# Kernel tuning notes

Hardware: AMD Instinct MI355X
Metric: run time of the kernel (lower is better)

## Reference

```python
import jax, jax.numpy as jnp
import numpy as np

LAYERS = 2      # LightGCN propagation layers
LAMB = 0.5      # aux loss weight
REG = 1e-4      # embedding reg weight
N_AUX = 2       # len(behaviors) - 1


def setup_inputs() -> dict:
    key = jax.random.key(0)
    k = jax.random.split(key, 8)
    n_users, n_items, d = 100000, 50000, 32
    E = 1000000
    user_emb = (jax.random.normal(k[0], (n_users + 1, d), jnp.float32) * 0.1).at[0].set(0.0)
    item_emb = (jax.random.normal(k[1], (n_items + 1, d), jnp.float32) * 0.1).at[0].set(0.0)
    aux_u = jax.random.randint(k[2], (N_AUX, E), 1, n_users + 1)
    aux_i = jax.random.randint(k[3], (N_AUX, E), 1, n_items + 1)
    aux_edges = jnp.stack([aux_u, aux_i], axis=-1).astype(jnp.int32)
    tgt_u = jax.random.randint(k[4], (E,), 1, n_users + 1)
    tgt_i = jax.random.randint(k[5], (E,), 1, n_items + 1)
    target_edges = jnp.stack([tgt_u, tgt_i], axis=-1).astype(jnp.int32)
    # [B, 1+N_AUX, 3]: per row (user, pos_item, neg_item) for target then each aux behavior
    batch_data = jax.random.randint(k[6], (4096, 1 + N_AUX, 3), 1, n_items + 1).astype(jnp.int32)
    return {"user_emb": user_emb, "item_emb": item_emb, "batch_data": batch_data,
            "aux_edges": aux_edges, "target_edges": target_edges}


def _graph(edges, n_user_rows, N):
    """Symmetric-normalized bipartite LightGCN graph as directed COO (src, dst, w)."""
    u = edges[:, 0]
    v = edges[:, 1] + n_user_rows  # shift item ids into joint node space
    ones = jnp.ones(u.shape[0], jnp.float32)
    deg = jax.ops.segment_sum(ones, u, num_segments=N) + jax.ops.segment_sum(ones, v, num_segments=N)
    dinv = jnp.where(deg > 0, jax.lax.rsqrt(jnp.maximum(deg, 1.0)), 0.0)
    w = dinv[u] * dinv[v]
    src = jnp.concatenate([u, v])
    dst = jnp.concatenate([v, u])
    w2 = jnp.concatenate([w, w])
    return src, dst, w2


def _lightgcn(emb, src, dst, w, N):
    """L-layer LightGCN propagation, mean over layers 0..L."""
    acc = emb
    cur = emb
    for _ in range(LAYERS):
        cur = jax.ops.segment_sum(w[:, None] * cur[src], dst, num_segments=N)
        acc = acc + cur
    return acc / (LAYERS + 1)


def _prob(ue, ie, u, i):
    return jax.nn.relu(jnp.sum(ue[u] * ie[i], axis=-1))


def _bpr(p, n):
    return -jnp.mean(jax.nn.log_sigmoid(p - n))


def reference(user_emb, item_emb, batch_data, aux_edges, target_edges):
    Nu = user_emb.shape[0]
    N = Nu + item_emb.shape[0]
    all_emb = jnp.concatenate([user_emb, item_emb], axis=0)
    tgt_g = _graph(target_edges, Nu, N)

    user, p_item, n_item = batch_data[:, 0, 0], batch_data[:, 0, 1], batch_data[:, 0, 2]
    aux_user, aux_p, aux_n = batch_data[:, 1:, 0], batch_data[:, 1:, 1], batch_data[:, 1:, 2]

    cps, cns, dps, dns, aps, ans, aux_losses = [], [], [], [], [], [], []
    for idx in range(N_AUX):
        # combine graph = aux behavior edges union target edges
        comb_edges = jnp.concatenate([aux_edges[idx], target_edges], axis=0)
        ce = _lightgcn(all_emb, *_graph(comb_edges, Nu, N), N)
        cu, ci = ce[:Nu], ce[Nu:]
        cps.append(_prob(cu, ci, user, p_item))
        cns.append(_prob(cu, ci, user, n_item))

        ae = _lightgcn(all_emb, *_graph(aux_edges[idx], Nu, N), N)
        au, ai = ae[:Nu], ae[Nu:]
        aps.append(_prob(au, ai, user, p_item))
        ans.append(_prob(au, ai, user, n_item))

        # condition: propagate aux embeddings through the target graph
        de = _lightgcn(ae, *tgt_g, N)
        du, di = de[:Nu], de[Nu:]
        dps.append(_prob(du, di, user, p_item))
        dns.append(_prob(du, di, user, n_item))

        ps = jnp.sum(au[aux_user[:, idx]] * ai[aux_p[:, idx]], axis=-1)
        ns = jnp.sum(au[aux_user[:, idx]] * ai[aux_n[:, idx]], axis=-1)
        aux_losses.append(_bpr(ps, ns))

    aux_loss = jnp.mean(jnp.stack(aux_losses))

    def front_door(cond, comb, aux):
        return jnp.sum(cond * jnp.sum(comb * aux, axis=0), axis=0)

    p_scores = front_door(jnp.stack(dps), jnp.stack(cps), jnp.stack(aps))
    n_scores = front_door(jnp.stack(dns), jnp.stack(cns), jnp.stack(ans))
    rec_loss = _bpr(p_scores, n_scores)
    emb_loss = (jnp.linalg.norm(user_emb) + jnp.linalg.norm(item_emb)) / item_emb.shape[0]
    return rec_loss + LAMB * aux_loss + REG * emb_loss
```

## Files before the change

### kernel.cpp

```cpp
#include <hip/hip_runtime.h>
#include <math.h>

#define D 32
#define ROWU 16
#define NBK 1024
#define BSHIFT 8
#define TILE_H 16384
#define TILE_BIN 2048
#define BCAP 7680

typedef unsigned int u32;
typedef unsigned short u16;

__device__ __forceinline__ float logsigf(float x) {
  return fminf(x, 0.f) - log1pf(expf(-fabsf(x)));
}

__device__ __forceinline__ float lo16(u32 u) { return __uint_as_float(u << 16); }
__device__ __forceinline__ float hi16(u32 u) { return __uint_as_float(u & 0xFFFF0000u); }
__device__ __forceinline__ u32 pk2(float a, float b) {
  u32 ua = __float_as_uint(a), ub = __float_as_uint(b);
  u32 ra = (ua + 0x7FFFu + ((ua >> 16) & 1u)) >> 16;
  u32 rb = (ub + 0x7FFFu + ((ub >> 16) & 1u)) >> 16;
  return (ra & 0xFFFFu) | (rb << 16);
}
__device__ __forceinline__ float bfat(const u16* __restrict__ p, size_t off) {
  return __uint_as_float(((u32)p[off]) << 16);
}
__device__ __forceinline__ void accum8(float* a, float w, uint4 x) {
  a[0] += w * lo16(x.x); a[1] += w * hi16(x.x);
  a[2] += w * lo16(x.y); a[3] += w * hi16(x.y);
  a[4] += w * lo16(x.z); a[5] += w * hi16(x.z);
  a[6] += w * lo16(x.w); a[7] += w * hi16(x.w);
}
__device__ __forceinline__ uint4 pack8(const float* a, float w) {
  return make_uint4(pk2(w * a[0], w * a[1]), pk2(w * a[2], w * a[3]),
                    pk2(w * a[4], w * a[5]), pk2(w * a[6], w * a[7]));
}


__global__ void hist_kernel(const int2* __restrict__ tgt, const int2* __restrict__ aux,
                            int E, int Nu, int BPS, int* __restrict__ bcur) {
  __shared__ int lh[NBK];
  int seg = blockIdx.x / BPS;
  int blk = blockIdx.x - seg * BPS;
  const int2* edges = (seg == 0) ? tgt : aux + (size_t)(seg - 1) * E;
  for (int b = threadIdx.x; b < NBK; b += 256) lh[b] = 0;
  __syncthreads();
  int e0 = blk * TILE_H;
  for (int k = threadIdx.x; k < TILE_H; k += 256) {
    int e = e0 + k;
    if (e < E) {
      int2 ed = edges[e];
      atomicAdd(&lh[ed.x >> BSHIFT], 1);
      atomicAdd(&lh[(ed.y + Nu) >> BSHIFT], 1);
    }
  }
  __syncthreads();
  for (int b = threadIdx.x; b < NBK; b += 256)
    if (lh[b]) atomicAdd(&bcur[seg * NBK + b], lh[b]);
}

__global__ void bscan_kernel(int* __restrict__ bcur) {
  int* b = bcur + blockIdx.x * NBK;
  int lane = threadIdx.x;
  int carry = 0;
  for (int base = 0; base < NBK; base += 64) {
    int i = base + lane;
    int v = b[i];
    int s = v;
    #pragma unroll
    for (int o = 1; o < 64; o <<= 1) {
      int t = __shfl_up(s, o);
      if (lane >= o) s += t;
    }
    b[i] = carry + s - v;
    carry += __shfl(s, 63);
  }
}

__global__ void bin_kernel(const int2* __restrict__ tgt, const int2* __restrict__ aux,
                           int E, int Nu, int BPS, int* __restrict__ bcur,
                           int* __restrict__ binned) {
  __shared__ int stage[2 * TILE_BIN];
  __shared__ int lh[NBK];
  __shared__ int loff[NBK];
  __shared__ int gb[NBK];
  __shared__ int wred[4];
  __shared__ int stot;
  int seg = blockIdx.x / BPS;
  int blk = blockIdx.x - seg * BPS;
  const int2* edges = (seg == 0) ? tgt : aux + (size_t)(seg - 1) * E;
  int* out = binned + (size_t)seg * 2 * E;
  int tid = threadIdx.x;
  for (int b = tid; b < NBK; b += 256) lh[b] = 0;
  __syncthreads();
  int e0 = blk * TILE_BIN;
  int pkv[16];
  int pb[16];
  int pr[16];
  #pragma unroll
  for (int it = 0; it < 8; ++it) {
    int e = e0 + tid + it * 256;
    bool ok = e < E;
    int2 ed = ok ? edges[e] : make_int2(0, -Nu);
    int u = ed.x, v = ed.y + Nu;
    int b1 = u >> BSHIFT, b2 = v >> BSHIFT;
    pkv[2 * it] = ((u & 255) << 18) | v;
    pb[2 * it] = b1;
    pr[2 * it] = ok ? atomicAdd(&lh[b1], 1) : 0;
    pkv[2 * it + 1] = ((v & 255) << 18) | u;
    pb[2 * it + 1] = b2;
    pr[2 * it + 1] = ok ? atomicAdd(&lh[b2], 1) : 0;
  }
  __syncthreads();
  int lane = tid & 63, wid = tid >> 6;
  int b4 = tid * 4;
  int v0 = lh[b4], v1 = lh[b4 + 1], v2 = lh[b4 + 2], v3 = lh[b4 + 3];
  int tsum = v0 + v1 + v2 + v3;
  int incl = tsum;
  #pragma unroll
  for (int o = 1; o < 64; o <<= 1) {
    int t = __shfl_up(incl, o);
    if (lane >= o) incl += t;
  }
  if (lane == 63) wred[wid] = incl;
  __syncthreads();
  int wbase = 0;
  for (int w = 0; w < wid; ++w) wbase += wred[w];
  int excl = wbase + incl - tsum;
  loff[b4] = excl;
  loff[b4 + 1] = excl + v0;
  loff[b4 + 2] = excl + v0 + v1;
  loff[b4 + 3] = excl + v0 + v1 + v2;
  if (tid == 255) stot = excl + tsum;
  #pragma unroll
  for (int j = 0; j < 4; ++j) {
    int b = b4 + j;
    int c = lh[b];
    gb[b] = c ? atomicAdd(&bcur[seg * NBK + b], c) : 0;
  }
  __syncthreads();
  #pragma unroll
  for (int it = 0; it < 16; ++it) {
    int e = e0 + tid + (it >> 1) * 256;
    if (e < E) stage[loff[pb[it]] + pr[it]] = pkv[it];
  }
  __syncthreads();
  int tot = stot;
  for (int k = tid; k < tot; k += 256) {
    int lo = 0, hi = NBK;
    while (lo < hi) {
      int mid = (lo + hi) >> 1;
      if (loff[mid] <= k) lo = mid + 1; else hi = mid;
    }
    int b = lo - 1;
    out[gb[b] + (k - loff[b])] = stage[k];
  }
}

__global__ void bucket_csr_kernel(const int* __restrict__ binned,
                                  const int* __restrict__ bend, int E2, int N, int NBKe,
                                  int* __restrict__ deg3, int* __restrict__ rp3,
                                  int* __restrict__ col_all) {
  __shared__ int ent[BCAP];
  __shared__ int cnt[256];
  __shared__ int off[256];
  __shared__ int wred[4];
  int seg = blockIdx.x / NBKe;
  int bkt = blockIdx.x - seg * NBKe;
  int node0 = bkt << BSHIFT;
  const int* bc = bend + seg * NBK;
  int start = (bkt == 0) ? 0 : bc[bkt - 1];
  int end = bc[bkt];
  int cntE = end - start;
  const int* src = binned + (size_t)seg * E2 + start;
  bool inLds = (cntE <= BCAP);
  if (inLds)
    for (int k = threadIdx.x; k < cntE; k += 256) ent[k] = src[k];
  cnt[threadIdx.x] = 0;
  __syncthreads();
  for (int k = threadIdx.x; k < cntE; k += 256) {
    int en = inLds ? ent[k] : src[k];
    atomicAdd(&cnt[en >> 18], 1);
  }
  __syncthreads();
  int lane = threadIdx.x & 63, wid = threadIdx.x >> 6;
  int v = cnt[threadIdx.x];
  int incl = v;
  #pragma unroll
  for (int o = 1; o < 64; o <<= 1) {
    int t = __shfl_up(incl, o);
    if (lane >= o) incl += t;
  }
  if (lane == 63) wred[wid] = incl;
  __syncthreads();
  int wbase = 0;
  for (int w = 0; w < wid; ++w) wbase += wred[w];
  off[threadIdx.x] = wbase + incl - v;
  int node = node0 + (int)threadIdx.x;
  if (node < N) {
    deg3[(size_t)seg * N + node] = v;
    rp3[(size_t)seg * (N + 1) + node] = start + wbase + incl - v;
  }
  if (bkt == 0 && threadIdx.x == 0) rp3[(size_t)seg * (N + 1) + N] = E2;
  __syncthreads();
  cnt[threadIdx.x] = 0;
  __syncthreads();
  int* col = col_all + (size_t)seg * E2 + start;
  for (int k = threadIdx.x; k < cntE; k += 256) {
    int en = inLds ? ent[k] : src[k];
    int lb = en >> 18;
    int pos = atomicAdd(&cnt[lb], 1);
    col[off[lb] + pos] = en & 0x3FFFF;
  }
}

__global__ void dinv_all_kernel(const int* __restrict__ deg3, float* __restrict__ dinv5,
                                int N) {
  int n = blockIdx.x * blockDim.x + threadIdx.x;
  if (n >= N) return;
  int dt = deg3[n], d0 = deg3[N + n], d1 = deg3[2 * N + n];
  dinv5[n]         = dt ? rsqrtf((float)dt) : 0.f;
  dinv5[N + n]     = d0 ? rsqrtf((float)d0) : 0.f;
  dinv5[2 * N + n] = d1 ? rsqrtf((float)d1) : 0.f;
  int c0 = dt + d0, c1 = dt + d1;
  dinv5[3 * N + n] = c0 ? rsqrtf((float)c0) : 0.f;
  dinv5[4 * N + n] = c1 ? rsqrtf((float)c1) : 0.f;
}

__global__ void cvt_emb_kernel(const float2* __restrict__ ue, long nu2,
                               const float2* __restrict__ ie, long ni2,
                               u32* __restrict__ emb) {
  long i = (long)blockIdx.x * blockDim.x + threadIdx.x;
  if (i >= nu2 + ni2) return;
  float2 v = (i < nu2) ? ue[i] : ie[i - nu2];
  emb[i] = pk2(v.x, v.y);
}


__global__ void gather_fused_all_kernel(const int* __restrict__ rp3,
                                        const int* __restrict__ col_all,
                                        const float* __restrict__ dinv5,
                                        const uint4* __restrict__ emb,
                                        uint4* __restrict__ BaAll, uint4* __restrict__ BcAll,
                                        int N, int E2) {
  const int* rpA0 = rp3 + (size_t)1 * (N + 1);
  const int* rpA1 = rp3 + (size_t)2 * (N + 1);
  const int* colA0 = col_all + (size_t)1 * E2;
  const int* colA1 = col_all + (size_t)2 * E2;
  const float* dvA0 = dinv5 + (size_t)1 * N;
  const float* dvA1 = dinv5 + (size_t)2 * N;
  const float* dvC0 = dinv5 + (size_t)3 * N;
  const float* dvC1 = dinv5 + (size_t)4 * N;
  int t = blockIdx.x * blockDim.x + threadIdx.x;
  int n = t >> 2;
  if (n >= N) return;
  int lane = t & 3;
  float aA0[8] = {0, 0, 0, 0, 0, 0, 0, 0};
  float aA1[8] = {0, 0, 0, 0, 0, 0, 0, 0};
  float aC0[8] = {0, 0, 0, 0, 0, 0, 0, 0};
  float aC1[8] = {0, 0, 0, 0, 0, 0, 0, 0};
  int s = rpA0[n], e = rpA0[n + 1];
  int j = s;
  for (; j + 1 < e; j += 2) {
    int c0 = colA0[j], c1 = colA0[j + 1];
    float wa0 = dvA0[c0], wc0 = dvC0[c0];
    float wa1 = dvA0[c1], wc1 = dvC0[c1];
    uint4 x0 = emb[(size_t)c0 * 4 + lane];
    uint4 x1 = emb[(size_t)c1 * 4 + lane];
    accum8(aA0, wa0, x0); accum8(aC0, wc0, x0);
    accum8(aA0, wa1, x1); accum8(aC0, wc1, x1);
  }
  if (j < e) {
    int c = colA0[j];
    float wa = dvA0[c], wc = dvC0[c];
    uint4 x = emb[(size_t)c * 4 + lane];
    accum8(aA0, wa, x); accum8(aC0, wc, x);
  }
  s = rpA1[n]; e = rpA1[n + 1];
  j = s;
  for (; j + 1 < e; j += 2) {
    int c0 = colA1[j], c1 = colA1[j + 1];
    float wa0 = dvA1[c0], wc0 = dvC1[c0];
    float wa1 = dvA1[c1], wc1 = dvC1[c1];
    uint4 x0 = emb[(size_t)c0 * 4 + lane];
    uint4 x1 = emb[(size_t)c1 * 4 + lane];
    accum8(aA1, wa0, x0); accum8(aC1, wc0, x0);
    accum8(aA1, wa1, x1); accum8(aC1, wc1, x1);
  }
  if (j < e) {
    int c = colA1[j];
    float wa = dvA1[c], wc = dvC1[c];
    uint4 x = emb[(size_t)c * 4 + lane];
    accum8(aA1, wa, x); accum8(aC1, wc, x);
  }
  s = rp3[n]; e = rp3[n + 1];
  j = s;
  for (; j + 1 < e; j += 2) {
    int c0 = col_all[j], c1 = col_all[j + 1];
    float w00 = dvC0[c0], w10 = dvC1[c0];
    float w01 = dvC0[c1], w11 = dvC1[c1];
    uint4 x0 = emb[(size_t)c0 * 4 + lane];
    uint4 x1 = emb[(size_t)c1 * 4 + lane];
    accum8(aC0, w00, x0); accum8(aC1, w10, x0);
    accum8(aC0, w01, x1); accum8(aC1, w11, x1);
  }
  if (j < e) {
    int c = col_all[j];
    float w0 = dvC0[c], w1 = dvC1[c];
    uint4 x = emb[(size_t)c * 4 + lane];
    accum8(aC0, w0, x); accum8(aC1, w1, x);
  }
  size_t o = (size_t)n * 4 + lane;
  size_t rowN4 = (size_t)N * 4;
  BaAll[o] = pack8(aA0, dvA0[n]);
  BaAll[rowN4 + o] = pack8(aA1, dvA1[n]);
  BcAll[o] = pack8(aC0, dvC0[n]);
  BcAll[rowN4 + o] = pack8(aC1, dvC1[n]);
}

__global__ void gather_avg_kernel(const int* __restrict__ rp3, const int* __restrict__ col_all,
                                  const float* __restrict__ dinv5,
                                  const uint4* __restrict__ emb,
                                  const uint4* __restrict__ BaAll, uint4* __restrict__ AAll,
                                  int N, int E2) {
  int idx = blockIdx.y;
  const int* rp = rp3 + (size_t)(1 + idx) * (N + 1);
  const int* col = col_all + (size_t)(1 + idx) * E2;
  const float* dv = dinv5 + (size_t)(1 + idx) * N;
  const uint4* cur = BaAll + (size_t)idx * N * 4;
  uint4* outA = AAll + (size_t)idx * N * 4;
  int t = blockIdx.x * blockDim.x + threadIdx.x;
  int n = t >> 2;
  if (n >= N) return;
  int lane = t & 3;
  float acc[8] = {0, 0, 0, 0, 0, 0, 0, 0};
  int s = rp[n], e = rp[n + 1];
  int j = s;
  for (; j + 1 < e; j += 2) {
    int c0 = col[j], c1 = col[j + 1];
    float w0 = dv[c0], w1 = dv[c1];
    uint4 x0 = cur[(size_t)c0 * 4 + lane];
    uint4 x1 = cur[(size_t)c1 * 4 + lane];
    accum8(acc, w0, x0);
    accum8(acc, w1, x1);
  }
  if (j < e) {
    int c = col[j];
    float w = dv[c];
    uint4 x = cur[(size_t)c * 4 + lane];
    accum8(acc, w, x);
  }
  float wn = dv[n];
  uint4 e4 = emb[(size_t)n * 4 + lane];
  uint4 b4 = cur[(size_t)n * 4 + lane];
  float r[8];
  r[0] = (lo16(e4.x) + lo16(b4.x) + wn * acc[0]) * (1.f / 3.f);
  r[1] = (hi16(e4.x) + hi16(b4.x) + wn * acc[1]) * (1.f / 3.f);
  r[2] = (lo16(e4.y) + lo16(b4.y) + wn * acc[2]) * (1.f / 3.f);
  r[3] = (hi16(e4.y) + hi16(b4.y) + wn * acc[3]) * (1.f / 3.f);
  r[4] = (lo16(e4.z) + lo16(b4.z) + wn * acc[4]) * (1.f / 3.f);
  r[5] = (hi16(e4.z) + hi16(b4.z) + wn * acc[5]) * (1.f / 3.f);
  r[6] = (lo16(e4.w) + lo16(b4.w) + wn * acc[6]) * (1.f / 3.f);
  r[7] = (hi16(e4.w) + hi16(b4.w) + wn * acc[7]) * (1.f / 3.f);
  outA[(size_t)n * 4 + lane] = pack8(r, 1.f);
}

__global__ void de_gather_kernel(const int* __restrict__ rp3, const int* __restrict__ col_all,
                                 const float* __restrict__ dinv5,
                                 const uint4* __restrict__ AAll, uint4* __restrict__ BaAll,
                                 int N, int E2) {
  int idx = blockIdx.y;
  const uint4* cur = AAll + (size_t)idx * N * 4;
  uint4* out = BaAll + (size_t)idx * N * 4;
  int t = blockIdx.x * blockDim.x + threadIdx.x;
  int n = t >> 2;
  if (n >= N) return;
  int lane = t & 3;
  float acc[8] = {0, 0, 0, 0, 0, 0, 0, 0};
  int s = rp3[n], e = rp3[n + 1];
  int j = s;
  for (; j + 1 < e; j += 2) {
    int c0 = col_all[j], c1 = col_all[j + 1];
    float w0 = dinv5[c0], w1 = dinv5[c1];
    uint4 x0 = cur[(size_t)c0 * 4 + lane];
    uint4 x1 = cur[(size_t)c1 * 4 + lane];
    accum8(acc, w0, x0);
    accum8(acc, w1, x1);
  }
  if (j < e) {
    int c = col_all[j];
    float w = dinv5[c];
    uint4 x = cur[(size_t)c * 4 + lane];
    accum8(acc, w, x);
  }
  out[(size_t)n * 4 + lane] = pack8(acc, dinv5[n]);
}


__device__ __forceinline__ float fdim2(const int* __restrict__ rpA, const int* __restrict__ colA,
                                       const int* __restrict__ rpT, const int* __restrict__ colT,
                                       const float* __restrict__ dv,
                                       const u16* __restrict__ base, const u16* __restrict__ L1,
                                       int r, int d) {
  float acc = 0.f;
  for (int j = rpA[r]; j < rpA[r + 1]; ++j) {
    int c = colA[j];
    acc += dv[c] * bfat(L1, (size_t)c * D + d);
  }
  if (colT != nullptr) {
    for (int j = rpT[r]; j < rpT[r + 1]; ++j) {
      int c = colT[j];
      acc += dv[c] * bfat(L1, (size_t)c * D + d);
    }
  }
  return (bfat(base, (size_t)r * D + d) + bfat(L1, (size_t)r * D + d) + dv[r] * acc) * (1.f / 3.f);
}

__global__ void ce_sparse_kernel(const int* __restrict__ rp3, const int* __restrict__ col_all,
                                 const float* __restrict__ dinv5,
                                 const u32* __restrict__ EMBu, const u32* __restrict__ BcAll,
                                 const int* __restrict__ batch, int Bsz, int Nu, int N, int E2,
                                 float* __restrict__ cps, float* __restrict__ cns) {
  int idx = blockIdx.y;
  const int* rpA = rp3 + (size_t)(1 + idx) * (N + 1);
  const int* colA = col_all + (size_t)(1 + idx) * E2;
  const float* dv = dinv5 + (size_t)(3 + idx) * N;
  const u16* base = (const u16*)EMBu;
  const u16* L1 = (const u16*)(BcAll + (size_t)idx * N * ROWU);
  float* outp = cps + (size_t)idx * Bsz;
  float* outn = cns + (size_t)idx * Bsz;
  int t = blockIdx.x * blockDim.x + threadIdx.x;
  int b = t >> 5, d = t & 31;
  if (b >= Bsz) return;
  int u = batch[b * 9 + 0];
  int p = batch[b * 9 + 1] + Nu;
  int n = batch[b * 9 + 2] + Nu;
  float uv = fdim2(rpA, colA, rp3, col_all, dv, base, L1, u, d);
  float pv = fdim2(rpA, colA, rp3, col_all, dv, base, L1, p, d);
  float nv = fdim2(rpA, colA, rp3, col_all, dv, base, L1, n, d);
  float sp = uv * pv, sn = uv * nv;
  #pragma unroll
  for (int o = 16; o > 0; o >>= 1) {
    sp += __shfl_down(sp, o, 32);
    sn += __shfl_down(sn, o, 32);
  }
  if (d == 0) {
    outp[b] = fmaxf(sp, 0.f);
    outn[b] = fmaxf(sn, 0.f);
  }
}

__global__ void de_sparse_kernel(const int* __restrict__ rp3, const int* __restrict__ col_all,
                                 const float* __restrict__ dinv5,
                                 const u32* __restrict__ AAll, const u32* __restrict__ BaAll,
                                 const int* __restrict__ batch, int Bsz, int Nu, int N, int E2,
                                 float* __restrict__ dps, float* __restrict__ dns) {
  int idx = blockIdx.y;
  const u16* base = (const u16*)(AAll + (size_t)idx * N * ROWU);
  const u16* L1 = (const u16*)(BaAll + (size_t)idx * N * ROWU);
  float* outp = dps + (size_t)idx * Bsz;
  float* outn = dns + (size_t)idx * Bsz;
  int t = blockIdx.x * blockDim.x + threadIdx.x;
  int b = t >> 5, d = t & 31;
  if (b >= Bsz) return;
  int u = batch[b * 9 + 0];
  int p = batch[b * 9 + 1] + Nu;
  int n = batch[b * 9 + 2] + Nu;
  float uv = fdim2(rp3, col_all, nullptr, nullptr, dinv5, base, L1, u, d);
  float pv = fdim2(rp3, col_all, nullptr, nullptr, dinv5, base, L1, p, d);
  float nv = fdim2(rp3, col_all, nullptr, nullptr, dinv5, base, L1, n, d);
  float sp = uv * pv, sn = uv * nv;
  #pragma unroll
  for (int o = 16; o > 0; o >>= 1) {
    sp += __shfl_down(sp, o, 32);
    sn += __shfl_down(sn, o, 32);
  }
  if (d == 0) {
    outp[b] = fmaxf(sp, 0.f);
    outn[b] = fmaxf(sn, 0.f);
  }
}


__device__ __forceinline__ float dotrow(const u32* __restrict__ a, const u32* __restrict__ b) {
  float s = 0.f;
  #pragma unroll
  for (int k = 0; k < ROWU; ++k) {
    u32 x = a[k], y = b[k];
    s += lo16(x) * lo16(y) + hi16(x) * hi16(y);
  }
  return s;
}

__global__ void score_aux_kernel(const u32* __restrict__ AAll, const int* __restrict__ batch,
                                 int Bsz, int Nu, int N, float* __restrict__ aps,
                                 float* __restrict__ ans_, float* __restrict__ accs) {
  int idx = blockIdx.y;
  const u32* A = AAll + (size_t)idx * N * ROWU;
  float* outp = aps + (size_t)idx * Bsz;
  float* outn = ans_ + (size_t)idx * Bsz;
  int b = blockIdx.x * blockDim.x + threadIdx.x;
  float l = 0.f;
  if (b < Bsz) {
    int u = batch[b * 9 + 0];
    int p = batch[b * 9 + 1] + Nu;
    int n = batch[b * 9 + 2] + Nu;
    const u32* ur = A + (size_t)u * ROWU;
    outp[b] = fmaxf(dotrow(ur, A + (size_t)p * ROWU), 0.f);
    outn[b] = fmaxf(dotrow(ur, A + (size_t)n * ROWU), 0.f);
    const int* r = batch + b * 9 + 3 * (1 + idx);
    const u32* aur = A + (size_t)r[0] * ROWU;
    float ps = dotrow(aur, A + (size_t)(r[1] + Nu) * ROWU);
    float ns = dotrow(aur, A + (size_t)(r[2] + Nu) * ROWU);
    l = -logsigf(ps - ns);
  }
  for (int o = 32; o > 0; o >>= 1) l += __shfl_down(l, o);
  if ((threadIdx.x & 63) == 0) atomicAdd(&accs[idx], l);
}

__global__ void recloss_kernel(const float* __restrict__ cps, const float* __restrict__ cns,
                               const float* __restrict__ aps, const float* __restrict__ ans_,
                               const float* __restrict__ dps, const float* __restrict__ dns,
                               int Bsz, int NA, float* __restrict__ acc) {
  int b = blockIdx.x * blockDim.x + threadIdx.x;
  float l = 0.f;
  if (b < Bsz) {
    float dp = 0.f, dn = 0.f, cap = 0.f, can = 0.f;
    for (int i = 0; i < NA; ++i) {
      dp += dps[i * Bsz + b];
      dn += dns[i * Bsz + b];
      cap += cps[i * Bsz + b] * aps[i * Bsz + b];
      can += cns[i * Bsz + b] * ans_[i * Bsz + b];
    }
    l = -logsigf(dp * cap - dn * can);
  }
  for (int o = 32; o > 0; o >>= 1) l += __shfl_down(l, o);
  if ((threadIdx.x & 63) == 0) atomicAdd(acc, l);
}

__global__ void sumsq2_kernel(const float4* __restrict__ xu, int n4u,
                              const float4* __restrict__ xi, int n4i,
                              float* __restrict__ accU, float* __restrict__ accI) {
  __shared__ float redU[4], redI[4];
  int tid = threadIdx.x;
  int gid = blockIdx.x * blockDim.x + tid;
  int stride = gridDim.x * blockDim.x;
  float su = 0.f, si = 0.f;
  for (int i = gid; i < n4u; i += stride) {
    float4 v = xu[i];
    su += v.x * v.x + v.y * v.y + v.z * v.z + v.w * v.w;
  }
  for (int i = gid; i < n4i; i += stride) {
    float4 v = xi[i];
    si += v.x * v.x + v.y * v.y + v.z * v.z + v.w * v.w;
  }
  for (int o = 32; o > 0; o >>= 1) {
    su += __shfl_down(su, o);
    si += __shfl_down(si, o);
  }
  if ((tid & 63) == 0) { redU[tid >> 6] = su; redI[tid >> 6] = si; }
  __syncthreads();
  if (tid == 0) {
    atomicAdd(accU, redU[0] + redU[1] + redU[2] + redU[3]);
    atomicAdd(accI, redI[0] + redI[1] + redI[2] + redI[3]);
  }
}

__global__ void final_kernel(const float* __restrict__ accs, int Bsz, int NA, int NiRows,
                             float* __restrict__ out) {
  float rec = accs[NA] / (float)Bsz;
  float aux = 0.f;
  for (int i = 0; i < NA; ++i) aux += accs[i] / (float)Bsz;
  aux /= (float)NA;
  float embl = (sqrtf(accs[NA + 1]) + sqrtf(accs[NA + 2])) / (float)NiRows;
  out[0] = rec + 0.5f * aux + 1e-4f * embl;
}

extern "C" void kernel_launch(void* const* d_in, const int* in_sizes, int n_in,
                              void* d_out, int out_size, void* d_ws, size_t ws_size,
                              hipStream_t stream) {
  const float* user_emb = (const float*)d_in[0];
  const float* item_emb = (const float*)d_in[1];
  const int* batch = (const int*)d_in[2];
  const int* aux_edges = (const int*)d_in[3];
  const int* tgt_edges = (const int*)d_in[4];

  const int NuRows = in_sizes[0] / D;
  const int NiRows = in_sizes[1] / D;
  const int Bsz = in_sizes[2] / 9;
  const int E = in_sizes[4] / 2;
  const int NA = in_sizes[3] / (2 * E);
  const int N = NuRows + NiRows;
  const int E2 = 2 * E;
  const size_t rowH = (size_t)N * ROWU;
  const int BPS_H = (E + TILE_H - 1) / TILE_H;
  const int BPS_B = (E + TILE_BIN - 1) / TILE_BIN;
  const int NBKe = (N + (1 << BSHIFT) - 1) >> BSHIFT;

  u32* EMBu = (u32*)d_ws;
  u32* AAll = EMBu + rowH;
  u32* BaAll = AAll + 2 * rowH;
  u32* BcAll = BaAll + 2 * rowH;
  int* deg3 = (int*)(BcAll + 2 * rowH);
  float* dinv5 = (float*)(deg3 + 3 * (size_t)N);
  int* rp3 = (int*)(dinv5 + 5 * (size_t)N);
  int* bcur = rp3 + 3 * (size_t)(N + 1);
  int* col_all = bcur + 3 * (size_t)NBK;
  float* cps = (float*)(col_all + 3 * (size_t)E2);
  float* cns = cps + (size_t)NA * Bsz;
  float* aps = cns + (size_t)NA * Bsz;
  float* ans_ = aps + (size_t)NA * Bsz;
  float* dps = ans_ + (size_t)NA * Bsz;
  float* dns = dps + (size_t)NA * Bsz;
  float* accs = dns + (size_t)NA * Bsz;
  int* binned = (int*)AAll;

  const int TB = 256;
  const int gN = (N + TB - 1) / TB;
  const int gN4 = (N * 4 + TB - 1) / TB;
  const int gB = (Bsz + TB - 1) / TB;
  const int gB32 = (Bsz * 32 + TB - 1) / TB;
  const long nu2 = (long)NuRows * ROWU;
  const long ni2 = (long)NiRows * ROWU;
  const int gCvt = (int)((nu2 + ni2 + TB - 1) / TB);

  cvt_emb_kernel<<<gCvt, TB, 0, stream>>>((const float2*)user_emb, nu2,
                                          (const float2*)item_emb, ni2, EMBu);

  hipMemsetAsync(bcur, 0, 3 * (size_t)NBK * sizeof(int), stream);
  hist_kernel<<<3 * BPS_H, TB, 0, stream>>>((const int2*)tgt_edges, (const int2*)aux_edges,
                                            E, NuRows, BPS_H, bcur);
  bscan_kernel<<<3, 64, 0, stream>>>(bcur);
  bin_kernel<<<3 * BPS_B, TB, 0, stream>>>((const int2*)tgt_edges, (const int2*)aux_edges,
                                           E, NuRows, BPS_B, bcur, binned);
  bucket_csr_kernel<<<3 * NBKe, TB, 0, stream>>>(binned, bcur, E2, N, NBKe,
                                                 deg3, rp3, col_all);
  dinv_all_kernel<<<gN, TB, 0, stream>>>(deg3, dinv5, N);

  hipMemsetAsync(accs, 0, (size_t)(NA + 3) * sizeof(float), stream);

  dim3 gridG(gN4, NA), gridB(gB, NA), gridS(gB32, NA);

  gather_fused_all_kernel<<<gN4, TB, 0, stream>>>(rp3, col_all, dinv5, (const uint4*)EMBu,
                                                  (uint4*)BaAll, (uint4*)BcAll, N, E2);
  gather_avg_kernel<<<gridG, TB, 0, stream>>>(rp3, col_all, dinv5, (const uint4*)EMBu,
                                              (const uint4*)BaAll, (uint4*)AAll, N, E2);
  score_aux_kernel<<<gridB, TB, 0, stream>>>(AAll, batch, Bsz, NuRows, N, aps, ans_, accs);
  ce_sparse_kernel<<<gridS, TB, 0, stream>>>(rp3, col_all, dinv5, EMBu, BcAll,
                                             batch, Bsz, NuRows, N, E2, cps, cns);
  de_gather_kernel<<<gridG, TB, 0, stream>>>(rp3, col_all, dinv5, (const uint4*)AAll,
                                             (uint4*)BaAll, N, E2);
  de_sparse_kernel<<<gridS, TB, 0, stream>>>(rp3, col_all, dinv5, AAll, BaAll,
                                             batch, Bsz, NuRows, N, E2, dps, dns);

  sumsq2_kernel<<<104, TB, 0, stream>>>((const float4*)user_emb,
                                        (int)((size_t)NuRows * D / 4),
                                        (const float4*)item_emb,
                                        (int)((size_t)NiRows * D / 4),
                                        accs + NA + 1, accs + NA + 2);
  recloss_kernel<<<gB, TB, 0, stream>>>(cps, cns, aps, ans_, dps, dns, Bsz, NA, accs + NA);
  final_kernel<<<1, 1, 0, stream>>>(accs, Bsz, NA, NiRows, (float*)d_out);
}
```

Measured before the change: 683.3 us.

## Interleave both aux embeddings per node and fuse de_gather across behaviors

The aux-propagated embeddings for both behaviors are now stored interleaved per node (64 bf16 per row), so the target-graph gather runs once with 8 lanes per node instead of once per behavior. The CSR column and weight lookups for the target graph are shared across both behaviors, and each neighbor fetch reads one contiguous 128-byte row. The gather_avg inner loop is also unrolled by four to put more loads in flight. Score and sparse kernels are updated to index the interleaved layout, at the cost of strided writes in gather_avg.

Measured after the change: 651.1 us. -4.7%, faster.

```diff
diff --git a/kernel.cpp b/kernel.cpp
--- a/kernel.cpp
+++ b/kernel.cpp
@@ -323,14 +323,13 @@
 __global__ void gather_avg_kernel(const int* __restrict__ rp3, const int* __restrict__ col_all,
                                   const float* __restrict__ dinv5,
                                   const uint4* __restrict__ emb,
-                                  const uint4* __restrict__ BaAll, uint4* __restrict__ AAll,
+                                  const uint4* __restrict__ BaAll, uint4* __restrict__ AI,
                                   int N, int E2) {
   int idx = blockIdx.y;
   const int* rp = rp3 + (size_t)(1 + idx) * (N + 1);
   const int* col = col_all + (size_t)(1 + idx) * E2;
   const float* dv = dinv5 + (size_t)(1 + idx) * N;
   const uint4* cur = BaAll + (size_t)idx * N * 4;
-  uint4* outA = AAll + (size_t)idx * N * 4;
   int t = blockIdx.x * blockDim.x + threadIdx.x;
   int n = t >> 2;
   if (n >= N) return;
@@ -338,15 +337,19 @@
   float acc[8] = {0, 0, 0, 0, 0, 0, 0, 0};
   int s = rp[n], e = rp[n + 1];
   int j = s;
-  for (; j + 1 < e; j += 2) {
-    int c0 = col[j], c1 = col[j + 1];
-    float w0 = dv[c0], w1 = dv[c1];
+  for (; j + 3 < e; j += 4) {
+    int c0 = col[j], c1 = col[j + 1], c2 = col[j + 2], c3 = col[j + 3];
+    float w0 = dv[c0], w1 = dv[c1], w2 = dv[c2], w3 = dv[c3];
     uint4 x0 = cur[(size_t)c0 * 4 + lane];
     uint4 x1 = cur[(size_t)c1 * 4 + lane];
+    uint4 x2 = cur[(size_t)c2 * 4 + lane];
+    uint4 x3 = cur[(size_t)c3 * 4 + lane];
     accum8(acc, w0, x0);
     accum8(acc, w1, x1);
-  }
-  if (j < e) {
+    accum8(acc, w2, x2);
+    accum8(acc, w3, x3);
+  }
+  for (; j < e; ++j) {
     int c = col[j];
     float w = dv[c];
     uint4 x = cur[(size_t)c * 4 + lane];
@@ -364,38 +367,35 @@
   r[5] = (hi16(e4.z) + hi16(b4.z) + wn * acc[5]) * (1.f / 3.f);
   r[6] = (lo16(e4.w) + lo16(b4.w) + wn * acc[6]) * (1.f / 3.f);
   r[7] = (hi16(e4.w) + hi16(b4.w) + wn * acc[7]) * (1.f / 3.f);
-  outA[(size_t)n * 4 + lane] = pack8(r, 1.f);
+  AI[(size_t)n * 8 + idx * 4 + lane] = pack8(r, 1.f);
 }
 
 __global__ void de_gather_kernel(const int* __restrict__ rp3, const int* __restrict__ col_all,
                                  const float* __restrict__ dinv5,
-                                 const uint4* __restrict__ AAll, uint4* __restrict__ BaAll,
-                                 int N, int E2) {
-  int idx = blockIdx.y;
-  const uint4* cur = AAll + (size_t)idx * N * 4;
-  uint4* out = BaAll + (size_t)idx * N * 4;
+                                 const uint4* __restrict__ AI, uint4* __restrict__ DeI,
+                                 int N) {
   int t = blockIdx.x * blockDim.x + threadIdx.x;
-  int n = t >> 2;
+  int n = t >> 3;
   if (n >= N) return;
-  int lane = t & 3;
+  int lane = t & 7;
   float acc[8] = {0, 0, 0, 0, 0, 0, 0, 0};
   int s = rp3[n], e = rp3[n + 1];
   int j = s;
   for (; j + 1 < e; j += 2) {
     int c0 = col_all[j], c1 = col_all[j + 1];
     float w0 = dinv5[c0], w1 = dinv5[c1];
-    uint4 x0 = cur[(size_t)c0 * 4 + lane];
-    uint4 x1 = cur[(size_t)c1 * 4 + lane];
+    uint4 x0 = AI[(size_t)c0 * 8 + lane];
+    uint4 x1 = AI[(size_t)c1 * 8 + lane];
     accum8(acc, w0, x0);
     accum8(acc, w1, x1);
   }
   if (j < e) {
     int c = col_all[j];
     float w = dinv5[c];
-    uint4 x = cur[(size_t)c * 4 + lane];
+    uint4 x = AI[(size_t)c * 8 + lane];
     accum8(acc, w, x);
   }
-  out[(size_t)n * 4 + lane] = pack8(acc, dinv5[n]);
+  DeI[(size_t)n * 8 + lane] = pack8(acc, dinv5[n]);
 }
 
 
@@ -409,13 +409,23 @@
     int c = colA[j];
     acc += dv[c] * bfat(L1, (size_t)c * D + d);
   }
-  if (colT != nullptr) {
-    for (int j = rpT[r]; j < rpT[r + 1]; ++j) {
-      int c = colT[j];
-      acc += dv[c] * bfat(L1, (size_t)c * D + d);
-    }
+  for (int j = rpT[r]; j < rpT[r + 1]; ++j) {
+    int c = colT[j];
+    acc += dv[c] * bfat(L1, (size_t)c * D + d);
   }
   return (bfat(base, (size_t)r * D + d) + bfat(L1, (size_t)r * D + d) + dv[r] * acc) * (1.f / 3.f);
+}
+
+__device__ __forceinline__ float fdim1i(const int* __restrict__ rp, const int* __restrict__ col,
+                                        const float* __restrict__ dv,
+                                        const u16* __restrict__ base, const u16* __restrict__ L1,
+                                        int r, int di) {
+  float acc = 0.f;
+  for (int j = rp[r]; j < rp[r + 1]; ++j) {
+    int c = col[j];
+    acc += dv[c] * bfat(L1, (size_t)c * 64 + di);
+  }
+  return (bfat(base, (size_t)r * 64 + di) + bfat(L1, (size_t)r * 64 + di) + dv[r] * acc) * (1.f / 3.f);
 }
 
 __global__ void ce_sparse_kernel(const int* __restrict__ rp3, const int* __restrict__ col_all,
@@ -454,23 +464,24 @@
 
 __global__ void de_sparse_kernel(const int* __restrict__ rp3, const int* __restrict__ col_all,
                                  const float* __restrict__ dinv5,
-                                 const u32* __restrict__ AAll, const u32* __restrict__ BaAll,
-                                 const int* __restrict__ batch, int Bsz, int Nu, int N, int E2,
+                                 const u32* __restrict__ AI, const u32* __restrict__ DeI,
+                                 const int* __restrict__ batch, int Bsz, int Nu, int N,
                                  float* __restrict__ dps, float* __restrict__ dns) {
   int idx = blockIdx.y;
-  const u16* base = (const u16*)(AAll + (size_t)idx * N * ROWU);
-  const u16* L1 = (const u16*)(BaAll + (size_t)idx * N * ROWU);
+  const u16* base = (const u16*)AI;
+  const u16* L1 = (const u16*)DeI;
   float* outp = dps + (size_t)idx * Bsz;
   float* outn = dns + (size_t)idx * Bsz;
   int t = blockIdx.x * blockDim.x + threadIdx.x;
   int b = t >> 5, d = t & 31;
   if (b >= Bsz) return;
+  int di = idx * 32 + d;
   int u = batch[b * 9 + 0];
   int p = batch[b * 9 + 1] + Nu;
   int n = batch[b * 9 + 2] + Nu;
-  float uv = fdim2(rp3, col_all, nullptr, nullptr, dinv5, base, L1, u, d);
-  float pv = fdim2(rp3, col_all, nullptr, nullptr, dinv5, base, L1, p, d);
-  float nv = fdim2(rp3, col_all, nullptr, nullptr, dinv5, base, L1, n, d);
+  float uv = fdim1i(rp3, col_all, dinv5, base, L1, u, di);
+  float pv = fdim1i(rp3, col_all, dinv5, base, L1, p, di);
+  float nv = fdim1i(rp3, col_all, dinv5, base, L1, n, di);
   float sp = uv * pv, sn = uv * nv;
   #pragma unroll
   for (int o = 16; o > 0; o >>= 1) {
@@ -494,11 +505,11 @@
   return s;
 }
 
-__global__ void score_aux_kernel(const u32* __restrict__ AAll, const int* __restrict__ batch,
+__global__ void score_aux_kernel(const u32* __restrict__ AI, const int* __restrict__ batch,
                                  int Bsz, int Nu, int N, float* __restrict__ aps,
                                  float* __restrict__ ans_, float* __restrict__ accs) {
   int idx = blockIdx.y;
-  const u32* A = AAll + (size_t)idx * N * ROWU;
+  const u32* A = AI + (size_t)idx * ROWU;
   float* outp = aps + (size_t)idx * Bsz;
   float* outn = ans_ + (size_t)idx * Bsz;
   int b = blockIdx.x * blockDim.x + threadIdx.x;
@@ -507,13 +518,13 @@
     int u = batch[b * 9 + 0];
     int p = batch[b * 9 + 1] + Nu;
     int n = batch[b * 9 + 2] + Nu;
-    const u32* ur = A + (size_t)u * ROWU;
-    outp[b] = fmaxf(dotrow(ur, A + (size_t)p * ROWU), 0.f);
-    outn[b] = fmaxf(dotrow(ur, A + (size_t)n * ROWU), 0.f);
+    const u32* ur = A + (size_t)u * 32;
+    outp[b] = fmaxf(dotrow(ur, A + (size_t)p * 32), 0.f);
+    outn[b] = fmaxf(dotrow(ur, A + (size_t)n * 32), 0.f);
     const int* r = batch + b * 9 + 3 * (1 + idx);
-    const u32* aur = A + (size_t)r[0] * ROWU;
-    float ps = dotrow(aur, A + (size_t)(r[1] + Nu) * ROWU);
-    float ns = dotrow(aur, A + (size_t)(r[2] + Nu) * ROWU);
+    const u32* aur = A + (size_t)r[0] * 32;
+    float ps = dotrow(aur, A + (size_t)(r[1] + Nu) * 32);
+    float ns = dotrow(aur, A + (size_t)(r[2] + Nu) * 32);
     l = -logsigf(ps - ns);
   }
   for (int o = 32; o > 0; o >>= 1) l += __shfl_down(l, o);
@@ -600,8 +611,8 @@
   const int NBKe = (N + (1 << BSHIFT) - 1) >> BSHIFT;
 
   u32* EMBu = (u32*)d_ws;
-  u32* AAll = EMBu + rowH;
-  u32* BaAll = AAll + 2 * rowH;
+  u32* AI = EMBu + rowH;
+  u32* BaAll = AI + 2 * rowH;
   u32* BcAll = BaAll + 2 * rowH;
   int* deg3 = (int*)(BcAll + 2 * rowH);
   float* dinv5 = (float*)(deg3 + 3 * (size_t)N);
@@ -615,11 +626,12 @@
   float* dps = ans_ + (size_t)NA * Bsz;
   float* dns = dps + (size_t)NA * Bsz;
   float* accs = dns + (size_t)NA * Bsz;
-  int* binned = (int*)AAll;
+  int* binned = (int*)AI;
 
   const int TB = 256;
   const int gN = (N + TB - 1) / TB;
   const int gN4 = (N * 4 + TB - 1) / TB;
+  const int gN8 = (N * 8 + TB - 1) / TB;
   const int gB = (Bsz + TB - 1) / TB;
   const int gB32 = (Bsz * 32 + TB - 1) / TB;
   const long nu2 = (long)NuRows * ROWU;
@@ -646,14 +658,14 @@
   gather_fused_all_kernel<<<gN4, TB, 0, stream>>>(rp3, col_all, dinv5, (const uint4*)EMBu,
                                                   (uint4*)BaAll, (uint4*)BcAll, N, E2);
   gather_avg_kernel<<<gridG, TB, 0, stream>>>(rp3, col_all, dinv5, (const uint4*)EMBu,
-                                              (const uint4*)BaAll, (uint4*)AAll, N, E2);
-  score_aux_kernel<<<gridB, TB, 0, stream>>>(AAll, batch, Bsz, NuRows, N, aps, ans_, accs);
+                                              (const uint4*)BaAll, (uint4*)AI, N, E2);
+  score_aux_kernel<<<gridB, TB, 0, stream>>>(AI, batch, Bsz, NuRows, N, aps, ans_, accs);
   ce_sparse_kernel<<<gridS, TB, 0, stream>>>(rp3, col_all, dinv5, EMBu, BcAll,
                                              batch, Bsz, NuRows, N, E2, cps, cns);
-  de_gather_kernel<<<gridG, TB, 0, stream>>>(rp3, col_all, dinv5, (const uint4*)AAll,
-                                             (uint4*)BaAll, N, E2);
-  de_sparse_kernel<<<gridS, TB, 0, stream>>>(rp3, col_all, dinv5, AAll, BaAll,
-                                             batch, Bsz, NuRows, N, E2, dps, dns);
+  de_gather_kernel<<<gN8, TB, 0, stream>>>(rp3, col_all, dinv5, (const uint4*)AI,
+                                           (uint4*)BaAll, N);
+  de_sparse_kernel<<<gridS, TB, 0, stream>>>(rp3, col_all, dinv5, AI, BaAll,
+                                             batch, Bsz, NuRows, N, dps, dns);
 
   sumsq2_kernel<<<104, TB, 0, stream>>>((const float4*)user_emb,
                                         (int)((size_t)NuRows * D / 4),
```
